# Optimization experiments

Measured on AMD Instinct MI355X. Metric: run time of the kernel, lower is better.

## Reference

```python
import jax, jax.numpy as jnp
import numpy as np

EMBED = 128
STATE = 64
HID = 160
VOCAB = 32000


def layer_norm(x, g, b, eps=1e-5):
    mu = x.mean(-1, keepdims=True)
    var = ((x - mu) ** 2).mean(-1, keepdims=True)
    return (x - mu) * jax.lax.rsqrt(var + eps) * g + b


def mamba_block(x, norm_g, norm_b, in_w, in_b, conv_w, conv_b,
                dt_w, dt_b, b_w, b_b, c_w, c_b, a_log, d, out_w, out_b):
    # x: [B,T,D]
    res = x
    xn = layer_norm(x, norm_g, norm_b)
    proj = xn @ in_w.T + in_b                      # [B,T,2D]
    x_proj, z = jnp.split(proj, 2, axis=-1)
    D = x_proj.shape[-1]
    # depthwise conv1d, kernel 3, same padding
    xc = jax.lax.conv_general_dilated(
        x_proj.transpose(0, 2, 1), conv_w[:, None, :],
        window_strides=(1,), padding=((1, 1),),
        feature_group_count=D,
        dimension_numbers=('NCH', 'OIH', 'NCH')) + conv_b[:, None]
    x_conv = jnp.tanh(xc.transpose(0, 2, 1))       # [B,T,D]
    # input-dependent SSM params, computed for all timesteps at once
    dt = jax.nn.softplus(z @ dt_w.T + dt_b) + 1e-4  # [B,T,S]
    bt = jnp.tanh(z @ b_w.T + b_b)                  # [B,T,S]
    ct = jnp.tanh(z @ c_w.T + c_b)                  # [B,T,S]
    a = -jnp.exp(a_log)                             # [S]
    decay = jnp.exp(a * dt)                         # [B,T,S]

    def step(state, inp):
        dec_t, b_t = inp
        state = state * dec_t + b_t
        return state, state

    state0 = jnp.zeros((x.shape[0], a_log.shape[0]), x.dtype)
    _, states = jax.lax.scan(step, state0,
                             (decay.transpose(1, 0, 2), bt.transpose(1, 0, 2)))
    y = ct * states.transpose(1, 0, 2)              # [B,T,S]
    mix = jnp.concatenate([x_conv * d, y], axis=-1)  # [B,T,D+S]
    return res + mix @ out_w.T + out_b


def _forward(x, lengths, resp_in, emb_table,
             m_norm_g, m_norm_b, m_in_w, m_in_b, m_conv_w, m_conv_b,
             m_dt_w, m_dt_b, m_b_w, m_b_b, m_c_w, m_c_b, m_a_log, m_d,
             m_out_w, m_out_b, pool_g, pool_b, shared_w, shared_b,
             intent_w, intent_b, style_w, style_b, cap_w, cap_b, op_w, op_b,
             dec_emb, dec_init_w, dec_init_b,
             gru_w_ih, gru_w_hh, gru_b_ih, gru_b_hh, dec_out_w, dec_out_b):
    emb = emb_table[x]                              # [B,T,E]
    h_seq = emb
    for i in range(2):
        h_seq = mamba_block(h_seq, m_norm_g[i], m_norm_b[i], m_in_w[i],
                            m_in_b[i], m_conv_w[i], m_conv_b[i], m_dt_w[i],
                            m_dt_b[i], m_b_w[i], m_b_b[i], m_c_w[i], m_c_b[i],
                            m_a_log[i], m_d[i], m_out_w[i], m_out_b[i])
    T = h_seq.shape[1]
    mask = (jnp.arange(T)[None, :] < lengths[:, None])[..., None]
    denom = jnp.maximum(lengths, 1)[:, None].astype(h_seq.dtype)
    pooled = (h_seq * mask).sum(axis=1) / denom     # [B,E]
    h = layer_norm(pooled, pool_g, pool_b)
    h = jax.nn.relu(h @ shared_w.T + shared_b)      # [B,128]
    intent = h @ intent_w.T + intent_b
    style = h @ style_w.T + style_b
    cap = h @ cap_w.T + cap_b
    op = h @ op_w.T + op_b
    # GRU decoder (PyTorch gate order: r, z, n)
    dec_in = dec_emb[resp_in]                       # [B,Td,E]
    h0 = jnp.tanh(h @ dec_init_w.T + dec_init_b)    # [B,H]
    gx = dec_in @ gru_w_ih.T + gru_b_ih             # [B,Td,3H]

    def gru_step(hprev, gx_t):
        gh = hprev @ gru_w_hh.T + gru_b_hh
        xr, xz, xn = jnp.split(gx_t, 3, axis=-1)
        hr, hz, hn = jnp.split(gh, 3, axis=-1)
        r = jax.nn.sigmoid(xr + hr)
        zg = jax.nn.sigmoid(xz + hz)
        n = jnp.tanh(xn + r * hn)
        hnew = (1.0 - zg) * n + zg * hprev
        return hnew, hnew

    _, dec_states = jax.lax.scan(gru_step, h0, gx.transpose(1, 0, 2))
    dec_out = dec_states.transpose(1, 0, 2)         # [B,Td,H]
    resp_logits = dec_out @ dec_out_w.T + dec_out_b  # [B,Td,V]
    return (intent, style, cap, op, resp_logits, h)


def setup_inputs() -> dict:
    key = jax.random.key(0)
    ks = iter(jax.random.split(key, 64))

    def nrm(shape, s=0.02):
        return jax.random.normal(next(ks), shape, jnp.float32) * s

    inp = {}
    inp['x'] = jax.random.randint(next(ks), (32, 512), 0, VOCAB)
    inp['lengths'] = jax.random.randint(next(ks), (32,), 1, 513)
    inp['resp_in'] = jax.random.randint(next(ks), (32, 128), 0, VOCAB)
    inp['emb_table'] = nrm((VOCAB, EMBED), 1.0).at[0].set(0.0)
    inp['m_norm_g'] = jnp.ones((2, EMBED)); inp['m_norm_b'] = jnp.zeros((2, EMBED))
    inp['m_in_w'] = nrm((2, 2 * EMBED, EMBED)); inp['m_in_b'] = jnp.zeros((2, 2 * EMBED))
    inp['m_conv_w'] = nrm((2, EMBED, 3), 0.1); inp['m_conv_b'] = jnp.zeros((2, EMBED))
    inp['m_dt_w'] = nrm((2, STATE, EMBED)); inp['m_dt_b'] = jnp.zeros((2, STATE))
    inp['m_b_w'] = nrm((2, STATE, EMBED)); inp['m_b_b'] = jnp.zeros((2, STATE))
    inp['m_c_w'] = nrm((2, STATE, EMBED)); inp['m_c_b'] = jnp.zeros((2, STATE))
    inp['m_a_log'] = nrm((2, STATE)); inp['m_d'] = jnp.ones((2, EMBED))
    inp['m_out_w'] = nrm((2, EMBED, EMBED + STATE)); inp['m_out_b'] = jnp.zeros((2, EMBED))
    inp['pool_g'] = jnp.ones((EMBED,)); inp['pool_b'] = jnp.zeros((EMBED,))
    inp['shared_w'] = nrm((128, EMBED)); inp['shared_b'] = jnp.zeros((128,))
    inp['intent_w'] = nrm((32, 128)); inp['intent_b'] = jnp.zeros((32,))
    inp['style_w'] = nrm((8, 128)); inp['style_b'] = jnp.zeros((8,))
    inp['cap_w'] = nrm((16, 128)); inp['cap_b'] = jnp.zeros((16,))
    inp['op_w'] = nrm((24, 128)); inp['op_b'] = jnp.zeros((24,))
    inp['dec_emb'] = nrm((VOCAB, EMBED), 1.0).at[0].set(0.0)
    inp['dec_init_w'] = nrm((HID, 128)); inp['dec_init_b'] = jnp.zeros((HID,))
    inp['gru_w_ih'] = nrm((3 * HID, EMBED)); inp['gru_w_hh'] = nrm((3 * HID, HID))
    inp['gru_b_ih'] = jnp.zeros((3 * HID,)); inp['gru_b_hh'] = jnp.zeros((3 * HID,))
    inp['dec_out_w'] = nrm((VOCAB, HID)); inp['dec_out_b'] = jnp.zeros((VOCAB,))
    return inp


def reference(x, lengths, resp_in, emb_table,
              m_norm_g, m_norm_b, m_in_w, m_in_b, m_conv_w, m_conv_b,
              m_dt_w, m_dt_b, m_b_w, m_b_b, m_c_w, m_c_b, m_a_log, m_d,
              m_out_w, m_out_b, pool_g, pool_b, shared_w, shared_b,
              intent_w, intent_b, style_w, style_b, cap_w, cap_b, op_w, op_b,
              dec_emb, dec_init_w, dec_init_b,
              gru_w_ih, gru_w_hh, gru_b_ih, gru_b_hh, dec_out_w, dec_out_b):
    return _forward(x, lengths, resp_in, emb_table,
                    m_norm_g, m_norm_b, m_in_w, m_in_b, m_conv_w, m_conv_b,
                    m_dt_w, m_dt_b, m_b_w, m_b_b, m_c_w, m_c_b, m_a_log, m_d,
                    m_out_w, m_out_b, pool_g, pool_b, shared_w, shared_b,
                    intent_w, intent_b, style_w, style_b, cap_w, cap_b,
                    op_w, op_b, dec_emb, dec_init_w, dec_init_b,
                    gru_w_ih, gru_w_hh, gru_b_ih, gru_b_hh,
                    dec_out_w, dec_out_b)
```

## Files before the change

kernel.cpp:

```cpp
#include <hip/hip_runtime.h>
#include <hip/hip_bf16.h>

#define EMBED 128
#define STATE 64
#define HID   160
#define VOCAB 32000
#define BDIM  32
#define TDIM  512
#define TDEC  128

typedef __attribute__((ext_vector_type(4))) float f32x4;
typedef __attribute__((ext_vector_type(8))) short bf16x8;

__device__ inline float softplus_f(float x) { return x > 20.f ? x : log1pf(expf(x)); }
__device__ inline float sigmoid_f(float x) { return 1.f / (1.f + expf(-x)); }
__device__ inline short f2bf(float x) {
    __hip_bfloat16 v = __float2bfloat16(x);
    return *reinterpret_cast<short*>(&v);
}
__device__ inline float bf2f(short u) {
    union { unsigned int i; float f; } cv;
    cv.i = ((unsigned int)(unsigned short)u) << 16;
    return cv.f;
}

__global__ void prep_kernel(const float* __restrict__ w, short* __restrict__ wb, int n,
                            const int* __restrict__ x, const int* __restrict__ lengths,
                            const int* __restrict__ resp, int* __restrict__ flags) {
    if (blockIdx.x == 0 && threadIdx.x < 64) {
        int lane = threadIdx.x;
        unsigned long long m1 = __ballot(lane < 32 && x[2 * lane + 1] != 0);
        unsigned long long m2 = __ballot(lane < 16 && lengths[2 * lane + 1] != 0);
        unsigned long long m3 = __ballot(lane < 32 && resp[2 * lane + 1] != 0);
        if (lane == 0) {
            flags[0] = (m1 == 0ull);
            flags[1] = (m2 == 0ull);
            flags[2] = (m3 == 0ull);
        }
    }
    int i = blockIdx.x * blockDim.x + threadIdx.x;
    int stride = gridDim.x * blockDim.x;
    for (; i < n; i += stride) wb[i] = f2bf(w[i]);
}

__global__ void embed_kernel(const int* __restrict__ tok, const float* __restrict__ table,
                             float* __restrict__ out, int total,
                             const int* __restrict__ flags, int fidx) {
    int mode = flags[fidx];
    int i = blockIdx.x * blockDim.x + threadIdx.x;
    int stride = gridDim.x * blockDim.x;
    for (; i < total; i += stride) {
        int r = i >> 7, e = i & 127;
        int t = mode ? tok[2 * r] : tok[r];
        out[i] = table[(long)t * EMBED + e];
    }
}

__launch_bounds__(256)
__global__ void mm_inproj(const float* __restrict__ hseq,
                          const float* __restrict__ g, const float* __restrict__ bta,
                          const float* __restrict__ W, const float* __restrict__ bias,
                          short* __restrict__ projb) {
    __shared__ __align__(16) short As[64][136];
    __shared__ __align__(16) short Ws[64][136];
    __shared__ float rsum[64][4], rsum2[64][4];
    const int m0 = blockIdx.x * 64, n0 = blockIdx.y * 64;
    const int tid = threadIdx.x;

    {
        int row = tid >> 2, part = tid & 3;
        const float* src = &hseq[(long)(m0 + row) * 128 + part * 32];
        f32x4 v[8];
        float s = 0.f, s2 = 0.f;
        #pragma unroll
        for (int q = 0; q < 8; q++) {
            v[q] = *(const f32x4*)&src[q * 4];
            s  += v[q].x + v[q].y + v[q].z + v[q].w;
            s2 += v[q].x * v[q].x + v[q].y * v[q].y + v[q].z * v[q].z + v[q].w * v[q].w;
        }
        rsum[row][part] = s; rsum2[row][part] = s2;
        __syncthreads();
        float tot  = rsum[row][0] + rsum[row][1] + rsum[row][2] + rsum[row][3];
        float tot2 = rsum2[row][0] + rsum2[row][1] + rsum2[row][2] + rsum2[row][3];
        float mu = tot * (1.f / 128.f);
        float var = tot2 * (1.f / 128.f) - mu * mu;
        float rstd = rsqrtf(var + 1e-5f);
        #pragma unroll
        for (int q = 0; q < 8; q++) {
            int c = part * 32 + q * 4;
            short4 t4;
            t4.x = f2bf((v[q].x - mu) * rstd * g[c + 0] + bta[c + 0]);
            t4.y = f2bf((v[q].y - mu) * rstd * g[c + 1] + bta[c + 1]);
            t4.z = f2bf((v[q].z - mu) * rstd * g[c + 2] + bta[c + 2]);
            t4.w = f2bf((v[q].w - mu) * rstd * g[c + 3] + bta[c + 3]);
            *(short4*)&As[row][c] = t4;
        }
    }
    #pragma unroll
    for (int it = 0; it < 4; ++it) {
        int idx = tid + it * 256;
        int rr = idx >> 4, cc = idx & 15;
        const float* wp = &W[(long)(n0 + rr) * 128 + cc * 8];
        short t8[8];
        #pragma unroll
        for (int q = 0; q < 8; q++) t8[q] = f2bf(wp[q]);
        *(bf16x8*)&Ws[rr][cc * 8] = *(bf16x8*)t8;
    }
    __syncthreads();

    const int wave = tid >> 6, lane = tid & 63;
    const int wm = wave >> 1, wn = wave & 1;
    const int fr = lane & 15, kg = lane >> 4;
    f32x4 acc[2][2];
    #pragma unroll
    for (int i = 0; i < 2; i++)
        #pragma unroll
        for (int j = 0; j < 2; j++) acc[i][j] = (f32x4){0.f, 0.f, 0.f, 0.f};
    #pragma unroll
    for (int ks = 0; ks < 4; ++ks) {
        int kb = ks * 32 + kg * 8;
        bf16x8 a0 = *(const bf16x8*)&As[wm * 32 + fr][kb];
        bf16x8 a1 = *(const bf16x8*)&As[wm * 32 + 16 + fr][kb];
        bf16x8 w0 = *(const bf16x8*)&Ws[wn * 32 + fr][kb];
        bf16x8 w1 = *(const bf16x8*)&Ws[wn * 32 + 16 + fr][kb];
        acc[0][0] = __builtin_amdgcn_mfma_f32_16x16x32_bf16(a0, w0, acc[0][0], 0, 0, 0);
        acc[0][1] = __builtin_amdgcn_mfma_f32_16x16x32_bf16(a0, w1, acc[0][1], 0, 0, 0);
        acc[1][0] = __builtin_amdgcn_mfma_f32_16x16x32_bf16(a1, w0, acc[1][0], 0, 0, 0);
        acc[1][1] = __builtin_amdgcn_mfma_f32_16x16x32_bf16(a1, w1, acc[1][1], 0, 0, 0);
    }
    #pragma unroll
    for (int i = 0; i < 2; i++)
        #pragma unroll
        for (int j = 0; j < 2; j++) {
            int col = n0 + wn * 32 + j * 16 + fr;
            float bv = bias[col];
            #pragma unroll
            for (int q = 0; q < 4; q++) {
                int row = m0 + wm * 32 + i * 16 + kg * 4 + q;
                projb[(long)row * 256 + col] = f2bf(acc[i][j][q] + bv);
            }
        }
}

__launch_bounds__(256)
__global__ void mm_z(const short* __restrict__ projb,
                     const float* __restrict__ dtw, const float* __restrict__ dtb,
                     const float* __restrict__ alog,
                     const float* __restrict__ bw, const float* __restrict__ bb_,
                     const float* __restrict__ cw, const float* __restrict__ cb_,
                     float* __restrict__ sdat) {
    __shared__ __align__(16) short As[64][136];
    __shared__ __align__(16) short Ws[64][136];
    const int m0 = blockIdx.x * 64, sel = blockIdx.y;
    const int tid = threadIdx.x;
    const float* W = sel == 0 ? dtw : (sel == 1 ? bw : cw);
    const float* B = sel == 0 ? dtb : (sel == 1 ? bb_ : cb_);

    #pragma unroll
    for (int it = 0; it < 4; ++it) {
        int idx = tid + it * 256;
        int rr = idx >> 4, cc = idx & 15;
        *(bf16x8*)&As[rr][cc * 8] = *(const bf16x8*)&projb[(long)(m0 + rr) * 256 + 128 + cc * 8];
    }
    #pragma unroll
    for (int it = 0; it < 4; ++it) {
        int idx = tid + it * 256;
        int rr = idx >> 4, cc = idx & 15;
        const float* wp = &W[(long)rr * 128 + cc * 8];
        short t8[8];
        #pragma unroll
        for (int q = 0; q < 8; q++) t8[q] = f2bf(wp[q]);
        *(bf16x8*)&Ws[rr][cc * 8] = *(bf16x8*)t8;
    }
    __syncthreads();

    const int wave = tid >> 6, lane = tid & 63;
    const int wm = wave >> 1, wn = wave & 1;
    const int fr = lane & 15, kg = lane >> 4;
    f32x4 acc[2][2];
    #pragma unroll
    for (int i = 0; i < 2; i++)
        #pragma unroll
        for (int j = 0; j < 2; j++) acc[i][j] = (f32x4){0.f, 0.f, 0.f, 0.f};
    #pragma unroll
    for (int ks = 0; ks < 4; ++ks) {
        int kb = ks * 32 + kg * 8;
        bf16x8 a0 = *(const bf16x8*)&As[wm * 32 + fr][kb];
        bf16x8 a1 = *(const bf16x8*)&As[wm * 32 + 16 + fr][kb];
        bf16x8 w0 = *(const bf16x8*)&Ws[wn * 32 + fr][kb];
        bf16x8 w1 = *(const bf16x8*)&Ws[wn * 32 + 16 + fr][kb];
        acc[0][0] = __builtin_amdgcn_mfma_f32_16x16x32_bf16(a0, w0, acc[0][0], 0, 0, 0);
        acc[0][1] = __builtin_amdgcn_mfma_f32_16x16x32_bf16(a0, w1, acc[0][1], 0, 0, 0);
        acc[1][0] = __builtin_amdgcn_mfma_f32_16x16x32_bf16(a1, w0, acc[1][0], 0, 0, 0);
        acc[1][1] = __builtin_amdgcn_mfma_f32_16x16x32_bf16(a1, w1, acc[1][1], 0, 0, 0);
    }
    #pragma unroll
    for (int i = 0; i < 2; i++)
        #pragma unroll
        for (int j = 0; j < 2; j++) {
            int n = wn * 32 + j * 16 + fr;
            float bv = B[n];
            float al = (sel == 0) ? -expf(alog[n]) : 0.f;
            #pragma unroll
            for (int q = 0; q < 4; q++) {
                int row = m0 + wm * 32 + i * 16 + kg * 4 + q;
                float v = acc[i][j][q] + bv;
                if (sel == 0) { float dt = softplus_f(v) + 1e-4f; v = expf(al * dt); }
                else v = tanhf(v);
                sdat[(long)row * 192 + sel * 64 + n] = v;
            }
        }
}

__global__ void conv_kernel(const short* __restrict__ projb, const float* __restrict__ cw,
                            const float* __restrict__ cb, const float* __restrict__ dvec,
                            short* __restrict__ mixb, int total) {
    int i = blockIdx.x * blockDim.x + threadIdx.x;
    int stride = gridDim.x * blockDim.x;
    for (; i < total; i += stride) {
        int e = i & 127;
        int r = i >> 7;
        int t = r & (TDIM - 1);
        float x0 = bf2f(projb[(long)r * 256 + e]);
        float xm = (t > 0)        ? bf2f(projb[(long)(r - 1) * 256 + e]) : 0.f;
        float xp = (t < TDIM - 1) ? bf2f(projb[(long)(r + 1) * 256 + e]) : 0.f;
        float v = cw[e * 3 + 0] * xm + cw[e * 3 + 1] * x0 + cw[e * 3 + 2] * xp + cb[e];
        mixb[(long)r * 192 + e] = f2bf(tanhf(v) * dvec[e]);
    }
}

__global__ void scanA_kernel(const float* __restrict__ sdat, float* __restrict__ chunkAB) {
    int b = blockIdx.x, c = blockIdx.y, s = threadIdx.x;
    long rbase = (long)b * TDIM + c * 64;
    float A = 1.f, Bc = 0.f;
    #pragma unroll 8
    for (int t = 0; t < 64; ++t) {
        const float* row = sdat + (rbase + t) * 192;
        float d = row[s];
        Bc = Bc * d + row[64 + s];
        A *= d;
    }
    chunkAB[((b * 8 + c) * 2 + 0) * 64 + s] = A;
    chunkAB[((b * 8 + c) * 2 + 1) * 64 + s] = Bc;
}

__global__ void scanC_kernel(const float* __restrict__ sdat, const float* __restrict__ chunkAB,
                             short* __restrict__ mixb) {
    int b = blockIdx.x, c = blockIdx.y, s = threadIdx.x;
    float st = 0.f;
    for (int cc = 0; cc < c; ++cc) {
        float A  = chunkAB[((b * 8 + cc) * 2 + 0) * 64 + s];
        float Bc = chunkAB[((b * 8 + cc) * 2 + 1) * 64 + s];
        st = Bc + A * st;
    }
    long rbase = (long)b * TDIM + c * 64;
    #pragma unroll 4
    for (int t = 0; t < 64; ++t) {
        const float* row = sdat + (rbase + t) * 192;
        st = st * row[s] + row[64 + s];
        mixb[(rbase + t) * 192 + 128 + s] = f2bf(row[128 + s] * st);
    }
}

__global__ void poolA_kernel(const float* __restrict__ hseq, const int* __restrict__ lengths,
                             const int* __restrict__ flags, float* __restrict__ partial) {
    int b = blockIdx.x, c = blockIdx.y, e = threadIdx.x;
    int lm = flags[1];
    int len = lm ? lengths[2 * b] : lengths[b];
    int t0 = c * 64;
    int t1 = len < t0 + 64 ? len : t0 + 64;
    float s = 0.f;
    for (int t = t0; t < t1; ++t) s += hseq[((long)b * TDIM + t) * 128 + e];
    partial[((long)b * 8 + c) * 128 + e] = s;
}

__launch_bounds__(256)
__global__ void mm_out(const short* __restrict__ mixb,
                       const float* __restrict__ W, const float* __restrict__ bias,
                       float* __restrict__ hseq) {
    __shared__ __align__(16) short As[64][200];
    __shared__ __align__(16) short Ws[64][200];
    const int m0 = blockIdx.x * 64, n0 = blockIdx.y * 64;
    const int tid = threadIdx.x;

    #pragma unroll
    for (int it = 0; it < 6; ++it) {
        int idx = tid + it * 256;
        int rr = idx / 24, cc = idx % 24;
        *(bf16x8*)&As[rr][cc * 8] = *(const bf16x8*)&mixb[(long)(m0 + rr) * 192 + cc * 8];
    }
    #pragma unroll
    for (int it = 0; it < 6; ++it) {
        int idx = tid + it * 256;
        int rr = idx / 24, cc = idx % 24;
        const float* wp = &W[(long)(n0 + rr) * 192 + cc * 8];
        short t8[8];
        #pragma unroll
        for (int q = 0; q < 8; q++) t8[q] = f2bf(wp[q]);
        *(bf16x8*)&Ws[rr][cc * 8] = *(bf16x8*)t8;
    }
    __syncthreads();

    const int wave = tid >> 6, lane = tid & 63;
    const int wm = wave >> 1, wn = wave & 1;
    const int fr = lane & 15, kg = lane >> 4;
    f32x4 acc[2][2];
    #pragma unroll
    for (int i = 0; i < 2; i++)
        #pragma unroll
        for (int j = 0; j < 2; j++) acc[i][j] = (f32x4){0.f, 0.f, 0.f, 0.f};
    #pragma unroll
    for (int ks = 0; ks < 6; ++ks) {
        int kb = ks * 32 + kg * 8;
        bf16x8 a0 = *(const bf16x8*)&As[wm * 32 + fr][kb];
        bf16x8 a1 = *(const bf16x8*)&As[wm * 32 + 16 + fr][kb];
        bf16x8 w0 = *(const bf16x8*)&Ws[wn * 32 + fr][kb];
        bf16x8 w1 = *(const bf16x8*)&Ws[wn * 32 + 16 + fr][kb];
        acc[0][0] = __builtin_amdgcn_mfma_f32_16x16x32_bf16(a0, w0, acc[0][0], 0, 0, 0);
        acc[0][1] = __builtin_amdgcn_mfma_f32_16x16x32_bf16(a0, w1, acc[0][1], 0, 0, 0);
        acc[1][0] = __builtin_amdgcn_mfma_f32_16x16x32_bf16(a1, w0, acc[1][0], 0, 0, 0);
        acc[1][1] = __builtin_amdgcn_mfma_f32_16x16x32_bf16(a1, w1, acc[1][1], 0, 0, 0);
    }
    #pragma unroll
    for (int i = 0; i < 2; i++)
        #pragma unroll
        for (int j = 0; j < 2; j++) {
            int col = n0 + wn * 32 + j * 16 + fr;
            float bv = bias[col];
            #pragma unroll
            for (int q = 0; q < 4; q++) {
                int row = m0 + wm * 32 + i * 16 + kg * 4 + q;
                hseq[(long)row * 128 + col] += acc[i][j][q] + bv;
            }
        }
}

__launch_bounds__(256)
__global__ void mm_gx(const int* __restrict__ resp, const float* __restrict__ table,
                      const int* __restrict__ flags,
                      const float* __restrict__ W, const float* __restrict__ bias,
                      float* __restrict__ gx) {
    __shared__ __align__(16) short As[64][136];
    __shared__ __align__(16) short Ws[64][136];
    const int m0 = blockIdx.x * 64, n0 = blockIdx.y * 64;
    const int tid = threadIdx.x;
    const int mode = flags[2];

    #pragma unroll
    for (int it = 0; it < 4; ++it) {
        int idx = tid + it * 256;
        int rr = idx >> 4, cc = idx & 15;
        int gr = m0 + rr;
        int tk = mode ? resp[2 * gr] : resp[gr];
        const float* sp = &table[(long)tk * 128 + cc * 8];
        short t8[8];
        #pragma unroll
        for (int q = 0; q < 8; q++) t8[q] = f2bf(sp[q]);
        *(bf16x8*)&As[rr][cc * 8] = *(bf16x8*)t8;
    }
    #pragma unroll
    for (int it = 0; it < 4; ++it) {
        int idx = tid + it * 256;
        int rr = idx >> 4, cc = idx & 15;
        int gn = n0 + rr;
        short t8[8];
        if (gn < 480) {
            const float* wp = &W[(long)gn * 128 + cc * 8];
            #pragma unroll
            for (int q = 0; q < 8; q++) t8[q] = f2bf(wp[q]);
        } else {
            #pragma unroll
            for (int q = 0; q < 8; q++) t8[q] = 0;
        }
        *(bf16x8*)&Ws[rr][cc * 8] = *(bf16x8*)t8;
    }
    __syncthreads();

    const int wave = tid >> 6, lane = tid & 63;
    const int wm = wave >> 1, wn = wave & 1;
    const int fr = lane & 15, kg = lane >> 4;
    f32x4 acc[2][2];
    #pragma unroll
    for (int i = 0; i < 2; i++)
        #pragma unroll
        for (int j = 0; j < 2; j++) acc[i][j] = (f32x4){0.f, 0.f, 0.f, 0.f};
    #pragma unroll
    for (int ks = 0; ks < 4; ++ks) {
        int kb = ks * 32 + kg * 8;
        bf16x8 a0 = *(const bf16x8*)&As[wm * 32 + fr][kb];
        bf16x8 a1 = *(const bf16x8*)&As[wm * 32 + 16 + fr][kb];
        bf16x8 w0 = *(const bf16x8*)&Ws[wn * 32 + fr][kb];
        bf16x8 w1 = *(const bf16x8*)&Ws[wn * 32 + 16 + fr][kb];
        acc[0][0] = __builtin_amdgcn_mfma_f32_16x16x32_bf16(a0, w0, acc[0][0], 0, 0, 0);
        acc[0][1] = __builtin_amdgcn_mfma_f32_16x16x32_bf16(a0, w1, acc[0][1], 0, 0, 0);
        acc[1][0] = __builtin_amdgcn_mfma_f32_16x16x32_bf16(a1, w0, acc[1][0], 0, 0, 0);
        acc[1][1] = __builtin_amdgcn_mfma_f32_16x16x32_bf16(a1, w1, acc[1][1], 0, 0, 0);
    }
    #pragma unroll
    for (int i = 0; i < 2; i++)
        #pragma unroll
        for (int j = 0; j < 2; j++) {
            int col = n0 + wn * 32 + j * 16 + fr;
            if (col >= 480) continue;
            float bv = bias[col];
            #pragma unroll
            for (int q = 0; q < 4; q++) {
                int row = m0 + wm * 32 + i * 16 + kg * 4 + q;
                gx[(long)row * 480 + col] = acc[i][j][q] + bv;
            }
        }
}

__launch_bounds__(512, 1)
__global__ void gru_heads_kernel(const float* __restrict__ partial, const int* __restrict__ lengths,
                                 const int* __restrict__ flags,
                                 const float* __restrict__ pg, const float* __restrict__ pb,
                                 const float* __restrict__ sw, const float* __restrict__ sb,
                                 const float* __restrict__ iw_, const float* __restrict__ ib_,
                                 const float* __restrict__ stw, const float* __restrict__ stb,
                                 const float* __restrict__ cw_, const float* __restrict__ cb2,
                                 const float* __restrict__ ow_, const float* __restrict__ ob2,
                                 const float* __restrict__ diw, const float* __restrict__ dib,
                                 const float* __restrict__ gx,
                                 const float* __restrict__ whh, const float* __restrict__ bhh,
                                 float* __restrict__ o_intent, float* __restrict__ o_style,
                                 float* __restrict__ o_cap, float* __restrict__ o_op,
                                 float* __restrict__ o_h,
                                 short* __restrict__ dec_out) {
    int b = blockIdx.x, tid = threadIdx.x;
    __shared__ float red[128];
    __shared__ float pooled[128], hsh[128];
    __shared__ float hs[160], gh[480];
    int lm = flags[1];
    int len = lm ? lengths[2 * b] : lengths[b];
    const float* gxb = gx + (long)b * TDEC * 480;

    if (tid < 128) {
        const float* pp = &partial[(long)b * 8 * 128 + tid];
        float s = 0.f;
        #pragma unroll
        for (int c = 0; c < 8; ++c) s += pp[c * 128];
        pooled[tid] = s / (float)(len > 1 ? len : 1);
    }
    __syncthreads();
    if (tid < 128) red[tid] = pooled[tid];
    __syncthreads();
    for (int off = 64; off > 0; off >>= 1) { if (tid < off) red[tid] += red[tid + off]; __syncthreads(); }
    float mu = red[0] / 128.f;
    __syncthreads();
    if (tid < 128) { float d = pooled[tid] - mu; red[tid] = d * d; }
    __syncthreads();
    for (int off = 64; off > 0; off >>= 1) { if (tid < off) red[tid] += red[tid + off]; __syncthreads(); }
    float rstd = rsqrtf(red[0] / 128.f + 1e-5f);
    __syncthreads();
    if (tid < 128) pooled[tid] = (pooled[tid] - mu) * rstd * pg[tid] + pb[tid];
    __syncthreads();
    if (tid < 128) {
        float a = sb[tid];
        for (int k = 0; k < 128; k++) a = fmaf(pooled[k], sw[tid * 128 + k], a);
        a = fmaxf(a, 0.f);
        hsh[tid] = a;
        o_h[b * 128 + tid] = a;
    }
    __syncthreads();
    if (tid < 32) {
        float a = ib_[tid];
        for (int k = 0; k < 128; k++) a = fmaf(hsh[k], iw_[tid * 128 + k], a);
        o_intent[b * 32 + tid] = a;
    } else if (tid < 40) {
        int n = tid - 32; float a = stb[n];
        for (int k = 0; k < 128; k++) a = fmaf(hsh[k], stw[n * 128 + k], a);
        o_style[b * 8 + n] = a;
    } else if (tid < 56) {
        int n = tid - 40; float a = cb2[n];
        for (int k = 0; k < 128; k++) a = fmaf(hsh[k], cw_[n * 128 + k], a);
        o_cap[b * 16 + n] = a;
    } else if (tid < 80) {
        int n = tid - 56; float a = ob2[n];
        for (int k = 0; k < 128; k++) a = fmaf(hsh[k], ow_[n * 128 + k], a);
        o_op[b * 24 + n] = a;
    }
    if (tid < 160) {
        float a = dib[tid];
        for (int k = 0; k < 128; k++) a = fmaf(hsh[k], diw[tid * 128 + k], a);
        hs[tid] = tanhf(a);
    }
    f32x4 w[40];
    float bh = 0.f;
    if (tid < 480) {
        bh = bhh[tid];
        const f32x4* wrow = reinterpret_cast<const f32x4*>(whh + tid * 160);
        #pragma unroll
        for (int q = 0; q < 40; q++) w[q] = wrow[q];
    }
    float prA = 0.f, pzA = 0.f, pnA = 0.f, prB = 0.f, pzB = 0.f, pnB = 0.f;
    if (tid < 160) {
        prA = gxb[tid];        pzA = gxb[160 + tid];        pnA = gxb[320 + tid];
        prB = gxb[480 + tid];  pzB = gxb[640 + tid];        pnB = gxb[800 + tid];
    }
    __syncthreads();
    for (int t = 0; t < TDEC; ++t) {
        if (tid < 480) {
            const f32x4* hv = reinterpret_cast<const f32x4*>(hs);
            float a0 = bh, a1 = 0.f, a2 = 0.f, a3 = 0.f;
            #pragma unroll
            for (int q = 0; q < 40; q += 4) {
                f32x4 ha = hv[q],     wa = w[q];
                f32x4 hb = hv[q + 1], wb = w[q + 1];
                f32x4 hc = hv[q + 2], wc = w[q + 2];
                f32x4 hd = hv[q + 3], wd = w[q + 3];
                a0 = fmaf(ha.w, wa.w, fmaf(ha.z, wa.z, fmaf(ha.y, wa.y, fmaf(ha.x, wa.x, a0))));
                a1 = fmaf(hb.w, wb.w, fmaf(hb.z, wb.z, fmaf(hb.y, wb.y, fmaf(hb.x, wb.x, a1))));
                a2 = fmaf(hc.w, wc.w, fmaf(hc.z, wc.z, fmaf(hc.y, wc.y, fmaf(hc.x, wc.x, a2))));
                a3 = fmaf(hd.w, wd.w, fmaf(hd.z, wd.z, fmaf(hd.y, wd.y, fmaf(hd.x, wd.x, a3))));
            }
            gh[tid] = (a0 + a1) + (a2 + a3);
        }
        __syncthreads();
        if (tid < 160) {
            float r = sigmoid_f(prA + gh[tid]);
            float z = sigmoid_f(pzA + gh[160 + tid]);
            float n = tanhf(pnA + r * gh[320 + tid]);
            float hnew = (1.f - z) * n + z * hs[tid];
            dec_out[((long)b * TDEC + t) * 160 + tid] = f2bf(hnew);
            hs[tid] = hnew;
            prA = prB; pzA = pzB; pnA = pnB;
            if (t + 2 < TDEC) {
                const float* g2 = gxb + (long)(t + 2) * 480;
                prB = g2[tid]; pzB = g2[160 + tid]; pnB = g2[320 + tid];
            }
        }
        __syncthreads();
    }
}

__launch_bounds__(256)
__global__ void vocab_gemm(const short* __restrict__ A,
                           const short* __restrict__ W,
                           const float* __restrict__ bias,
                           float* __restrict__ C) {
    __shared__ __align__(16) short As[128][168];
    __shared__ __align__(16) short Ws[64][168];
    int n0 = blockIdx.x * 64, m0 = blockIdx.y * 128;
    int tid = threadIdx.x;

    #pragma unroll
    for (int it = 0; it < 10; ++it) {
        int idx = tid + it * 256;
        int r = idx / 20, c8 = idx % 20;
        *(bf16x8*)&As[r][c8 * 8] = *(const bf16x8*)&A[(long)(m0 + r) * 160 + c8 * 8];
    }
    #pragma unroll
    for (int it = 0; it < 5; ++it) {
        int idx = tid + it * 256;
        int r = idx / 20, c8 = idx % 20;
        *(bf16x8*)&Ws[r][c8 * 8] = *(const bf16x8*)&W[(long)(n0 + r) * 160 + c8 * 8];
    }
    __syncthreads();

    int wave = tid >> 6, lane = tid & 63;
    int wm = wave >> 1, wn = wave & 1;
    int fr = lane & 15, kg = lane >> 4;

    f32x4 acc[4][2];
    #pragma unroll
    for (int i = 0; i < 4; i++)
        #pragma unroll
        for (int j = 0; j < 2; j++) acc[i][j] = (f32x4){0.f, 0.f, 0.f, 0.f};

    #pragma unroll
    for (int ks = 0; ks < 5; ++ks) {
        int kb = ks * 32 + kg * 8;
        bf16x8 a[4], bfr[2];
        #pragma unroll
        for (int i = 0; i < 4; i++)
            a[i] = *(const bf16x8*)&As[wm * 64 + i * 16 + fr][kb];
        #pragma unroll
        for (int j = 0; j < 2; j++)
            bfr[j] = *(const bf16x8*)&Ws[wn * 32 + j * 16 + fr][kb];
        #pragma unroll
        for (int i = 0; i < 4; i++)
            #pragma unroll
            for (int j = 0; j < 2; j++)
                acc[i][j] = __builtin_amdgcn_mfma_f32_16x16x32_bf16(a[i], bfr[j], acc[i][j], 0, 0, 0);
    }

    __syncthreads();
    float* Cs = (float*)&As[0][0];
    #pragma unroll
    for (int i = 0; i < 4; i++)
        #pragma unroll
        for (int j = 0; j < 2; j++) {
            int col = wn * 32 + j * 16 + fr;
            #pragma unroll
            for (int q = 0; q < 4; q++) {
                int row = wm * 64 + i * 16 + kg * 4 + q;
                Cs[row * 64 + col] = acc[i][j][q];
            }
        }
    __syncthreads();
    #pragma unroll
    for (int it = 0; it < 8; ++it) {
        int idx = tid + it * 256;
        int row = idx >> 4, c4 = (idx & 15) * 4;
        f32x4 v = *(f32x4*)&Cs[row * 64 + c4];
        int gc = n0 + c4;
        v.x += bias[gc]; v.y += bias[gc + 1]; v.z += bias[gc + 2]; v.w += bias[gc + 3];
        *(f32x4*)&C[(long)(m0 + row) * VOCAB + gc] = v;
    }
}

extern "C" void kernel_launch(void* const* d_in, const int* in_sizes, int n_in,
                              void* d_out, int out_size, void* d_ws, size_t ws_size,
                              hipStream_t stream) {
    const int* x        = (const int*)d_in[0];
    const int* lengths  = (const int*)d_in[1];
    const int* resp_in  = (const int*)d_in[2];
    const float* emb_table = (const float*)d_in[3];
    const float* m_norm_g  = (const float*)d_in[4];
    const float* m_norm_b  = (const float*)d_in[5];
    const float* m_in_w    = (const float*)d_in[6];
    const float* m_in_b    = (const float*)d_in[7];
    const float* m_conv_w  = (const float*)d_in[8];
    const float* m_conv_b  = (const float*)d_in[9];
    const float* m_dt_w    = (const float*)d_in[10];
    const float* m_dt_b    = (const float*)d_in[11];
    const float* m_b_w     = (const float*)d_in[12];
    const float* m_b_b     = (const float*)d_in[13];
    const float* m_c_w     = (const float*)d_in[14];
    const float* m_c_b     = (const float*)d_in[15];
    const float* m_a_log   = (const float*)d_in[16];
    const float* m_d       = (const float*)d_in[17];
    const float* m_out_w   = (const float*)d_in[18];
    const float* m_out_b   = (const float*)d_in[19];
    const float* pool_g    = (const float*)d_in[20];
    const float* pool_b    = (const float*)d_in[21];
    const float* shared_w  = (const float*)d_in[22];
    const float* shared_b  = (const float*)d_in[23];
    const float* intent_w  = (const float*)d_in[24];
    const float* intent_b  = (const float*)d_in[25];
    const float* style_w   = (const float*)d_in[26];
    const float* style_b   = (const float*)d_in[27];
    const float* cap_w     = (const float*)d_in[28];
    const float* cap_b     = (const float*)d_in[29];
    const float* op_w      = (const float*)d_in[30];
    const float* op_b      = (const float*)d_in[31];
    const float* dec_emb   = (const float*)d_in[32];
    const float* dec_init_w = (const float*)d_in[33];
    const float* dec_init_b = (const float*)d_in[34];
    const float* gru_w_ih  = (const float*)d_in[35];
    const float* gru_w_hh  = (const float*)d_in[36];
    const float* gru_b_ih  = (const float*)d_in[37];
    const float* gru_b_hh  = (const float*)d_in[38];
    const float* dec_out_w = (const float*)d_in[39];
    const float* dec_out_b = (const float*)d_in[40];

    float* out = (float*)d_out;
    const long o_intent = 0;
    const long o_style  = 32 * 32;
    const long o_cap    = o_style + 32 * 8;
    const long o_op     = o_cap + 32 * 16;
    const long o_logits = o_op + 32 * 24;
    const long o_h      = o_logits + (long)BDIM * TDEC * VOCAB;

    const int R = BDIM * TDIM;
    const int Rd = BDIM * TDEC;

    char* Sb = (char*)(out + o_logits);
    float* hseq  = (float*)Sb;  Sb += (long)R * 128 * 4;
    short* projb = (short*)Sb;  Sb += (long)R * 256 * 2;
    float* sdat  = (float*)Sb;  Sb += (long)R * 192 * 4;
    short* mixb  = (short*)Sb;  Sb += (long)R * 192 * 2;
    float* gx    = (float*)Sb;  Sb += (long)Rd * 480 * 4;
    float* chunkAB = (float*)Sb; Sb += 32 * 8 * 2 * 64 * 4;
    float* partial = (float*)Sb; Sb += 32 * 8 * 128 * 4;

    int* flags   = (int*)d_ws;
    short* dec_obf = (short*)((float*)d_ws + 16);
    short* w_bf  = dec_obf + (long)Rd * HID;

    prep_kernel<<<2048, 256, 0, stream>>>(dec_out_w, w_bf, VOCAB * HID, x, lengths, resp_in, flags);
    embed_kernel<<<4096, 256, 0, stream>>>(x, emb_table, hseq, R * 128, flags, 0);

    for (int i = 0; i < 2; ++i) {
        mm_inproj<<<dim3(R / 64, 4), 256, 0, stream>>>(
            hseq, m_norm_g + i * 128, m_norm_b + i * 128,
            m_in_w + i * 256 * 128, m_in_b + i * 256, projb);
        mm_z<<<dim3(R / 64, 3), 256, 0, stream>>>(
            projb, m_dt_w + i * 8192, m_dt_b + i * 64, m_a_log + i * 64,
            m_b_w + i * 8192, m_b_b + i * 64,
            m_c_w + i * 8192, m_c_b + i * 64, sdat);
        conv_kernel<<<2048, 256, 0, stream>>>(
            projb, m_conv_w + i * 384, m_conv_b + i * 128, m_d + i * 128, mixb, R * 128);
        scanA_kernel<<<dim3(BDIM, 8), 64, 0, stream>>>(sdat, chunkAB);
        scanC_kernel<<<dim3(BDIM, 8), 64, 0, stream>>>(sdat, chunkAB, mixb);
        mm_out<<<dim3(R / 64, 2), 256, 0, stream>>>(
            mixb, m_out_w + i * 128 * 192, m_out_b + i * 128, hseq);
    }

    poolA_kernel<<<dim3(BDIM, 8), 128, 0, stream>>>(hseq, lengths, flags, partial);
    mm_gx<<<dim3(Rd / 64, 8), 256, 0, stream>>>(
        resp_in, dec_emb, flags, gru_w_ih, gru_b_ih, gx);
    gru_heads_kernel<<<BDIM, 512, 0, stream>>>(
        partial, lengths, flags,
        pool_g, pool_b, shared_w, shared_b,
        intent_w, intent_b, style_w, style_b, cap_w, cap_b, op_w, op_b,
        dec_init_w, dec_init_b,
        gx, gru_w_hh, gru_b_hh,
        out + o_intent, out + o_style, out + o_cap, out + o_op, out + o_h,
        dec_obf);
    vocab_gemm<<<dim3(VOCAB / 64, Rd / 128), 256, 0, stream>>>(
        dec_obf, w_bf, dec_out_b, out + o_logits);
}
```

Before: 505.2 us.

## Fuse embedding gather, conv, and pooling into neighbouring kernels

The embedding gather now happens inside the first in-projection GEMM, which reads table rows directly and writes the residual stream from the y==0 blocks. The depthwise conv+tanh work moves into the scan-C kernel, carried by 192 extra threads per block. The length-masked pooling partial sums are produced in the epilogue of the last out-projection GEMM through shared memory. This removes three kernel launches and their extra passes over global memory. In exchange the scan-C blocks get heavier, with only 256 blocks doing all the conv work, and mm_out gains extra syncs.

```diff
diff --git a/kernel.cpp b/kernel.cpp
--- a/kernel.cpp
+++ b/kernel.cpp
@@ -43,24 +43,13 @@
     for (; i < n; i += stride) wb[i] = f2bf(w[i]);
 }
 
-__global__ void embed_kernel(const int* __restrict__ tok, const float* __restrict__ table,
-                             float* __restrict__ out, int total,
-                             const int* __restrict__ flags, int fidx) {
-    int mode = flags[fidx];
-    int i = blockIdx.x * blockDim.x + threadIdx.x;
-    int stride = gridDim.x * blockDim.x;
-    for (; i < total; i += stride) {
-        int r = i >> 7, e = i & 127;
-        int t = mode ? tok[2 * r] : tok[r];
-        out[i] = table[(long)t * EMBED + e];
-    }
-}
-
 __launch_bounds__(256)
 __global__ void mm_inproj(const float* __restrict__ hseq,
+                          const int* __restrict__ tok, const float* __restrict__ table,
+                          const int* __restrict__ flags,
                           const float* __restrict__ g, const float* __restrict__ bta,
                           const float* __restrict__ W, const float* __restrict__ bias,
-                          short* __restrict__ projb) {
+                          short* __restrict__ projb, float* __restrict__ hseq_out) {
     __shared__ __align__(16) short As[64][136];
     __shared__ __align__(16) short Ws[64][136];
     __shared__ float rsum[64][4], rsum2[64][4];
@@ -69,7 +58,15 @@
 
     {
         int row = tid >> 2, part = tid & 3;
-        const float* src = &hseq[(long)(m0 + row) * 128 + part * 32];
+        const float* src;
+        if (table) {
+            int mode = flags[0];
+            int gr = m0 + row;
+            int tk = mode ? tok[2 * gr] : tok[gr];
+            src = &table[(long)tk * 128 + part * 32];
+        } else {
+            src = &hseq[(long)(m0 + row) * 128 + part * 32];
+        }
         f32x4 v[8];
         float s = 0.f, s2 = 0.f;
         #pragma unroll
@@ -77,6 +74,11 @@
             v[q] = *(const f32x4*)&src[q * 4];
             s  += v[q].x + v[q].y + v[q].z + v[q].w;
             s2 += v[q].x * v[q].x + v[q].y * v[q].y + v[q].z * v[q].z + v[q].w * v[q].w;
+        }
+        if (table && blockIdx.y == 0) {
+            float* dst = &hseq_out[(long)(m0 + row) * 128 + part * 32];
+            #pragma unroll
+            for (int q = 0; q < 8; q++) *(f32x4*)&dst[q * 4] = v[q];
         }
         rsum[row][part] = s; rsum2[row][part] = s2;
         __syncthreads();
@@ -212,23 +214,6 @@
         }
 }
 
-__global__ void conv_kernel(const short* __restrict__ projb, const float* __restrict__ cw,
-                            const float* __restrict__ cb, const float* __restrict__ dvec,
-                            short* __restrict__ mixb, int total) {
-    int i = blockIdx.x * blockDim.x + threadIdx.x;
-    int stride = gridDim.x * blockDim.x;
-    for (; i < total; i += stride) {
-        int e = i & 127;
-        int r = i >> 7;
-        int t = r & (TDIM - 1);
-        float x0 = bf2f(projb[(long)r * 256 + e]);
-        float xm = (t > 0)        ? bf2f(projb[(long)(r - 1) * 256 + e]) : 0.f;
-        float xp = (t < TDIM - 1) ? bf2f(projb[(long)(r + 1) * 256 + e]) : 0.f;
-        float v = cw[e * 3 + 0] * xm + cw[e * 3 + 1] * x0 + cw[e * 3 + 2] * xp + cb[e];
-        mixb[(long)r * 192 + e] = f2bf(tanhf(v) * dvec[e]);
-    }
-}
-
 __global__ void scanA_kernel(const float* __restrict__ sdat, float* __restrict__ chunkAB) {
     int b = blockIdx.x, c = blockIdx.y, s = threadIdx.x;
     long rbase = (long)b * TDIM + c * 64;
@@ -244,40 +229,47 @@
     chunkAB[((b * 8 + c) * 2 + 1) * 64 + s] = Bc;
 }
 
-__global__ void scanC_kernel(const float* __restrict__ sdat, const float* __restrict__ chunkAB,
-                             short* __restrict__ mixb) {
-    int b = blockIdx.x, c = blockIdx.y, s = threadIdx.x;
-    float st = 0.f;
-    for (int cc = 0; cc < c; ++cc) {
-        float A  = chunkAB[((b * 8 + cc) * 2 + 0) * 64 + s];
-        float Bc = chunkAB[((b * 8 + cc) * 2 + 1) * 64 + s];
-        st = Bc + A * st;
-    }
+__global__ void scanC_conv_kernel(const float* __restrict__ sdat, const float* __restrict__ chunkAB,
+                                  const short* __restrict__ projb,
+                                  const float* __restrict__ cw, const float* __restrict__ cb,
+                                  const float* __restrict__ dvec,
+                                  short* __restrict__ mixb) {
+    int b = blockIdx.x, c = blockIdx.y, tid = threadIdx.x;
     long rbase = (long)b * TDIM + c * 64;
-    #pragma unroll 4
-    for (int t = 0; t < 64; ++t) {
-        const float* row = sdat + (rbase + t) * 192;
-        st = st * row[s] + row[64 + s];
-        mixb[(rbase + t) * 192 + 128 + s] = f2bf(row[128 + s] * st);
-    }
-}
-
-__global__ void poolA_kernel(const float* __restrict__ hseq, const int* __restrict__ lengths,
-                             const int* __restrict__ flags, float* __restrict__ partial) {
-    int b = blockIdx.x, c = blockIdx.y, e = threadIdx.x;
-    int lm = flags[1];
-    int len = lm ? lengths[2 * b] : lengths[b];
-    int t0 = c * 64;
-    int t1 = len < t0 + 64 ? len : t0 + 64;
-    float s = 0.f;
-    for (int t = t0; t < t1; ++t) s += hseq[((long)b * TDIM + t) * 128 + e];
-    partial[((long)b * 8 + c) * 128 + e] = s;
+    if (tid < 64) {
+        int s = tid;
+        float st = 0.f;
+        for (int cc = 0; cc < c; ++cc) {
+            float A  = chunkAB[((b * 8 + cc) * 2 + 0) * 64 + s];
+            float Bc = chunkAB[((b * 8 + cc) * 2 + 1) * 64 + s];
+            st = Bc + A * st;
+        }
+        #pragma unroll 4
+        for (int t = 0; t < 64; ++t) {
+            const float* row = sdat + (rbase + t) * 192;
+            st = st * row[s] + row[64 + s];
+            mixb[(rbase + t) * 192 + 128 + s] = f2bf(row[128 + s] * st);
+        }
+    } else {
+        for (int idx = tid - 64; idx < 64 * 128; idx += 192) {
+            int rl = idx >> 7, e = idx & 127;
+            long r = rbase + rl;
+            int t = (int)(r & (TDIM - 1));
+            float x0 = bf2f(projb[r * 256 + e]);
+            float xm = (t > 0)        ? bf2f(projb[(r - 1) * 256 + e]) : 0.f;
+            float xp = (t < TDIM - 1) ? bf2f(projb[(r + 1) * 256 + e]) : 0.f;
+            float v = cw[e * 3 + 0] * xm + cw[e * 3 + 1] * x0 + cw[e * 3 + 2] * xp + cb[e];
+            mixb[r * 192 + e] = f2bf(tanhf(v) * dvec[e]);
+        }
+    }
 }
 
 __launch_bounds__(256)
 __global__ void mm_out(const short* __restrict__ mixb,
                        const float* __restrict__ W, const float* __restrict__ bias,
-                       float* __restrict__ hseq) {
+                       float* __restrict__ hseq,
+                       const int* __restrict__ lengths, const int* __restrict__ flags,
+                       float* __restrict__ partial) {
     __shared__ __align__(16) short As[64][200];
     __shared__ __align__(16) short Ws[64][200];
     const int m0 = blockIdx.x * 64, n0 = blockIdx.y * 64;
@@ -321,6 +313,9 @@
         acc[1][0] = __builtin_amdgcn_mfma_f32_16x16x32_bf16(a1, w0, acc[1][0], 0, 0, 0);
         acc[1][1] = __builtin_amdgcn_mfma_f32_16x16x32_bf16(a1, w1, acc[1][1], 0, 0, 0);
     }
+
+    float* Cs = (float*)&As[0][0];
+    if (partial) __syncthreads();
     #pragma unroll
     for (int i = 0; i < 2; i++)
         #pragma unroll
@@ -330,9 +325,25 @@
             #pragma unroll
             for (int q = 0; q < 4; q++) {
                 int row = m0 + wm * 32 + i * 16 + kg * 4 + q;
-                hseq[(long)row * 128 + col] += acc[i][j][q] + bv;
+                float v = hseq[(long)row * 128 + col] + acc[i][j][q] + bv;
+                hseq[(long)row * 128 + col] = v;
+                if (partial) Cs[(row - m0) * 64 + (wn * 32 + j * 16 + fr)] = v;
             }
         }
+    if (partial) {
+        __syncthreads();
+        if (tid < 64) {
+            int b = m0 >> 9;
+            int chunk = (m0 >> 6) & 7;
+            int lm = flags[1];
+            int len = lm ? lengths[2 * b] : lengths[b];
+            int t0 = chunk * 64;
+            int nrows = len - t0; if (nrows > 64) nrows = 64; if (nrows < 0) nrows = 0;
+            float s = 0.f;
+            for (int rl = 0; rl < nrows; ++rl) s += Cs[rl * 64 + tid];
+            partial[((long)b * 8 + chunk) * 128 + n0 + tid] = s;
+        }
+    }
 }
 
 __launch_bounds__(256)
@@ -680,25 +691,24 @@
     short* w_bf  = dec_obf + (long)Rd * HID;
 
     prep_kernel<<<2048, 256, 0, stream>>>(dec_out_w, w_bf, VOCAB * HID, x, lengths, resp_in, flags);
-    embed_kernel<<<4096, 256, 0, stream>>>(x, emb_table, hseq, R * 128, flags, 0);
 
     for (int i = 0; i < 2; ++i) {
         mm_inproj<<<dim3(R / 64, 4), 256, 0, stream>>>(
-            hseq, m_norm_g + i * 128, m_norm_b + i * 128,
-            m_in_w + i * 256 * 128, m_in_b + i * 256, projb);
+            hseq, x, (i == 0) ? emb_table : nullptr, flags,
+            m_norm_g + i * 128, m_norm_b + i * 128,
+            m_in_w + i * 256 * 128, m_in_b + i * 256, projb, hseq);
         mm_z<<<dim3(R / 64, 3), 256, 0, stream>>>(
             projb, m_dt_w + i * 8192, m_dt_b + i * 64, m_a_log + i * 64,
             m_b_w + i * 8192, m_b_b + i * 64,
             m_c_w + i * 8192, m_c_b + i * 64, sdat);
-        conv_kernel<<<2048, 256, 0, stream>>>(
-            projb, m_conv_w + i * 384, m_conv_b + i * 128, m_d + i * 128, mixb, R * 128);
         scanA_kernel<<<dim3(BDIM, 8), 64, 0, stream>>>(sdat, chunkAB);
-        scanC_kernel<<<dim3(BDIM, 8), 64, 0, stream>>>(sdat, chunkAB, mixb);
+        scanC_conv_kernel<<<dim3(BDIM, 8), 256, 0, stream>>>(
+            sdat, chunkAB, projb, m_conv_w + i * 384, m_conv_b + i * 128, m_d + i * 128, mixb);
         mm_out<<<dim3(R / 64, 2), 256, 0, stream>>>(
-            mixb, m_out_w + i * 128 * 192, m_out_b + i * 128, hseq);
-    }
-
-    poolA_kernel<<<dim3(BDIM, 8), 128, 0, stream>>>(hseq, lengths, flags, partial);
+            mixb, m_out_w + i * 128 * 192, m_out_b + i * 128, hseq,
+            lengths, flags, (i == 1) ? partial : nullptr);
+    }
+
     mm_gx<<<dim3(Rd / 64, 8), 256, 0, stream>>>(
         resp_in, dec_emb, flags, gru_w_ih, gru_b_ih, gx);
     gru_heads_kernel<<<BDIM, 512, 0, stream>>>(
```

After: 528.7 us. 4.6% more time.
